# Kernel optimization log

Hardware: AMD Instinct MI355X
Metric: run time of the kernel (lower is better)

Reference implementation:

```python
import jax, jax.numpy as jnp
import numpy as np

B, T, D = 4096, 64, 64
NE, NR = 100000, 100
PREFIXES = ["kgi", "ddp", "kgp", "ddo", "kgi1", "ddp1", "kgp1", "ddo1"]


def setup_inputs() -> dict:
    key = jax.random.key(0)
    keys = iter(jax.random.split(key, 80))
    inp = {"items": jax.random.randint(next(keys), (B,), 0, NE)}
    for p in PREFIXES:
        for s, hi in [("h0", NE), ("h1", NE), ("r0", NR), ("r1", NR), ("t0", NE), ("t1", NE)]:
            inp[p + "_" + s] = jax.random.randint(next(keys), (B, T), 0, hi)
    inp["embeddings_0"] = jax.random.normal(next(keys), (B, D), jnp.float32)
    inp["embeddings_1"] = jax.random.normal(next(keys), (B, D), jnp.float32)
    inp["entity_emb"] = jax.random.normal(next(keys), (NE, D), jnp.float32) * 0.05
    inp["relation_emb"] = jax.random.normal(next(keys), (NR, D), jnp.float32) * 0.05
    inp["W1"] = jax.random.normal(next(keys), (2 * D, D), jnp.float32) * (1.0 / np.sqrt(2 * D))
    inp["W2"] = jax.random.normal(next(keys), (D, 1), jnp.float32) * (1.0 / np.sqrt(D))
    return inp


def _knowledge_attention(h_set, path, t, W1, W2):
    # h_set, path, t: [B, T, D]; tiny sigmoid MLP -> softmax over triples -> weighted sum
    x = jnp.concatenate([h_set, path], axis=-1)                 # [B, T, 2D]
    att = jax.nn.sigmoid(jax.nn.sigmoid(x @ W1) @ W2)[..., 0]   # [B, T]
    att = jax.nn.softmax(att, axis=-1)
    return jnp.einsum('bt,btd->bd', att, t)                     # [B, D]


def _layers(E, R, W1, W2, h0, h1, r0, r1, t0, t1, init):
    # Faithful to the original n_layer=2 loop:
    #  i=0: h=E[h0], p=R[r0], t=E[t0];  i=1: h=E[h0]+E[h1], p=R[r0]*R[r1], t=E[t1]
    embs = [init]
    h, p = E[h0], R[r0]
    embs.append(_knowledge_attention(h, p, E[t0], W1, W2))
    h = h + E[h1]
    p = p * R[r1]
    embs.append(_knowledge_attention(h, p, E[t1], W1, W2))
    return embs


def reference(items, kgi_h0, kgi_h1, kgi_r0, kgi_r1, kgi_t0, kgi_t1,
              ddp_h0, ddp_h1, ddp_r0, ddp_r1, ddp_t0, ddp_t1,
              kgp_h0, kgp_h1, kgp_r0, kgp_r1, kgp_t0, kgp_t1,
              ddo_h0, ddo_h1, ddo_r0, ddo_r1, ddo_t0, ddo_t1,
              kgi1_h0, kgi1_h1, kgi1_r0, kgi1_r1, kgi1_t0, kgi1_t1,
              ddp1_h0, ddp1_h1, ddp1_r0, ddp1_r1, ddp1_t0, ddp1_t1,
              kgp1_h0, kgp1_h1, kgp1_r0, kgp1_r1, kgp1_t0, kgp1_t1,
              ddo1_h0, ddo1_h1, ddo1_r0, ddo1_r1, ddo1_t0, ddo1_t1,
              embeddings_0, embeddings_1, entity_emb, relation_emb, W1, W2):
    E, R = entity_emb, relation_emb
    kg = _layers(E, R, W1, W2, kgi_h0, kgi_h1, kgi_r0, kgi_r1, kgi_t0, kgi_t1, E[kgi_h0].mean(1))
    ddi = _layers(E, R, W1, W2, ddp_h0, ddp_h1, ddp_r0, ddp_r1, ddp_t0, ddp_t1, E[items])
    kgp = _layers(E, R, W1, W2, kgp_h0, kgp_h1, kgp_r0, kgp_r1, kgp_t0, kgp_t1, E[kgp_h0].mean(1))
    ddo = _layers(E, R, W1, W2, ddo_h0, ddo_h1, ddo_r0, ddo_r1, ddo_t0, ddo_t1, E[ddo_h0].mean(1))
    kg1 = _layers(E, R, W1, W2, kgi1_h0, kgi1_h1, kgi1_r0, kgi1_r1, kgi1_t0, kgi1_t1, E[kgi1_h0].mean(1))
    ddi1 = _layers(E, R, W1, W2, ddp1_h0, ddp1_h1, ddp1_r0, ddp1_r1, ddp1_t0, ddp1_t1, E[ddp1_h0].mean(1))
    kgp1 = _layers(E, R, W1, W2, kgp1_h0, kgp1_h1, kgp1_r0, kgp1_r1, kgp1_t0, kgp1_t1, E[kgp1_h0].mean(1))
    ddo1 = _layers(E, R, W1, W2, ddo1_h0, ddo1_h1, ddo1_r0, ddo1_r1, ddo1_t0, ddo1_t1, E[ddo1_h0].mean(1))
    del ddo, kg1, kgp1  # dead in the original score due to list aliasing/overwrite in predict()
    # predict() with agg='concat'; original aliases ddi_origin_embeddings = ddi_embeddings,
    drug_kg = [jnp.concatenate([kg[i], ddi[i]], -1) for i in range(3)]       # [B, 2D]
    drug_kg2 = [jnp.concatenate([kgp[i], ddi[i]], -1) for i in range(3)]     # [B, 2D]
    drug_d = [jnp.concatenate([ddi1[i], ddo1[i]], -1) for i in range(3)]     # [B, 2D]
    e_u = jnp.concatenate([drug_kg[2], drug_kg[1], drug_kg[0]], -1)          # [B, 6D]
    e_p_u = jnp.concatenate([drug_kg2[2], drug_kg2[1], drug_kg2[0]], -1)     # [B, 6D]
    e_i = jnp.concatenate([drug_d[2], drug_d[1], drug_d[0]], -1)             # [B, 6D]
    e1 = jnp.concatenate([e_u, e_p_u], -1)                                   # [B, 12D]
    e2 = jnp.concatenate([e_i, e_i], -1)                                     # [B, 12D] (e_p_i aliases e_i)
    scores = jax.nn.sigmoid(jnp.sum(e1 * e2, axis=-1))                       # [B]
    return scores
```

## Files before the change

### kernel.cpp

```cpp
#include <hip/hip_runtime.h>

#define BATCH 4096
#define NE 100000

typedef __attribute__((ext_vector_type(8))) short bf16x8;
typedef __attribute__((ext_vector_type(4))) float f32x4;

union U4 { uint4 u4; bf16x8 v; };

struct GPtrs {
    const int* h0[5]; const int* h1[5];
    const int* r0[5]; const int* r1[5];
    const int* t0[5]; const int* t1[5];
};

__device__ __forceinline__ unsigned trunc2(float lo, float hi){
    return __builtin_amdgcn_perm(__float_as_uint(hi), __float_as_uint(lo), 0x07060302u);
}
__device__ __forceinline__ float bflo(unsigned u){ return __uint_as_float(u << 16); }
__device__ __forceinline__ float bfhi(unsigned u){ return __uint_as_float(u & 0xFFFF0000u); }
__device__ __forceinline__ float bf2f(unsigned short h){ return __uint_as_float(((unsigned)h) << 16); }
__device__ __forceinline__ unsigned addw(unsigned x, unsigned y){
    return trunc2(bflo(x)+bflo(y), bfhi(x)+bfhi(y));
}
__device__ __forceinline__ unsigned mulw(unsigned x, unsigned y){
    return trunc2(bflo(x)*bflo(y), bfhi(x)*bfhi(y));
}
__device__ __forceinline__ float sigm(float x){ return __builtin_amdgcn_rcpf(1.0f + __expf(-x)); }

__global__ __launch_bounds__(256)
void prep_kernel(const float* __restrict__ E, const float* __restrict__ R,
                 const float* __restrict__ W1,
                 unsigned short* __restrict__ ebf, unsigned short* __restrict__ rbf,
                 uint4* __restrict__ w1pk)
{
    const int EC = (NE*64)/8;
    const int RC = (100*64)/8;
    const int WC = 1024;
    int stride = gridDim.x * blockDim.x;
    for (int c = blockIdx.x*blockDim.x + threadIdx.x; c < EC + RC + WC; c += stride) {
        if (c < EC + RC) {
            const float* src; unsigned short* dst;
            if (c < EC) { src = E + c*8;      dst = ebf + c*8; }
            else        { src = R + (c-EC)*8; dst = rbf + (c-EC)*8; }
            float4 a = *(const float4*)src;
            float4 b = *(const float4*)(src + 4);
            uint4 o;
            o.x = trunc2(a.x,a.y); o.y = trunc2(a.z,a.w);
            o.z = trunc2(b.x,b.y); o.w = trunc2(b.z,b.w);
            *(uint4*)dst = o;
        } else {
            int c2   = c - (EC + RC);
            int frag = c2 >> 6;
            int ln   = c2 & 63;
            int row  = (frag >> 2)*16 + (ln & 15);
            int kp0  = (frag & 3)*16 + 4*(ln >> 4);
            uint4 o;
            o.x = trunc2(W1[(2*kp0    )*64 + row], W1[(2*kp0 + 1)*64 + row]);
            o.y = trunc2(W1[(2*kp0 + 2)*64 + row], W1[(2*kp0 + 3)*64 + row]);
            o.z = trunc2(W1[(2*kp0 + 4)*64 + row], W1[(2*kp0 + 5)*64 + row]);
            o.w = trunc2(W1[(2*kp0 + 6)*64 + row], W1[(2*kp0 + 7)*64 + row]);
            w1pk[c2] = o;
        }
    }
}

__global__ __launch_bounds__(256, 2)
void group_kernel(GPtrs gp, const int* __restrict__ items,
                  const float* __restrict__ E,
                  const unsigned short* __restrict__ ebf,
                  const unsigned short* __restrict__ rbf,
                  const uint4* __restrict__ w1pk, const float* __restrict__ W2,
                  float* __restrict__ ws)
{
    const int g    = blockIdx.y;
    const int b    = blockIdx.x;
    const int tid  = threadIdx.x;
    const int lane = tid & 63;
    const int wv   = tid >> 6;

    __shared__ uint4 wlds[1024];
    __shared__ float red_log[64];
    __shared__ float red_pv[4][64];

    {
        wlds[tid      ] = w1pk[tid      ];
        wlds[tid + 256] = w1pk[tid + 256];
        wlds[tid + 512] = w1pk[tid + 512];
        wlds[tid + 768] = w1pk[tid + 768];
    }

    const int tcol = lane & 15;
    const int q    = lane >> 4;
    const int q4   = q * 4;
    const int t_   = wv*16 + tcol;

    int vh0 = gp.h0[g][b*64 + lane];
    int vh1 = gp.h1[g][b*64 + lane];
    int vr0 = gp.r0[g][b*64 + lane];
    int vr1 = gp.r1[g][b*64 + lane];
    int vt0 = gp.t0[g][b*64 + lane];
    int vt1 = gp.t1[g][b*64 + lane];

    __syncthreads();

    if (g == 1) {
        if (wv == 0) ws[((g*3 + 0)*BATCH + b)*64 + lane] = E[items[b]*64 + lane];
    } else {
        float o0 = 0.f, o1 = 0.f, o2 = 0.f, o3 = 0.f;
        #pragma unroll
        for (int u = 0; u < 16; u += 4) {
            int t = wv*16 + u;
            int r0_ = __shfl(vh0, t,   64);
            int r1_ = __shfl(vh0, t+1, 64);
            int r2_ = __shfl(vh0, t+2, 64);
            int r3_ = __shfl(vh0, t+3, 64);
            o0 += bf2f(ebf[r0_*64 + lane]); o1 += bf2f(ebf[r1_*64 + lane]);
            o2 += bf2f(ebf[r2_*64 + lane]); o3 += bf2f(ebf[r3_*64 + lane]);
        }
        red_pv[wv][lane] = ((o0+o1)+(o2+o3));
        __syncthreads();
        if (wv == 0)
            ws[((g*3 + 0)*BATCH + b)*64 + lane] =
                (red_pv[0][lane]+red_pv[1][lane]+red_pv[2][lane]+red_pv[3][lane]) * (1.0f/64.0f);
    }

    U4 f0, f1, f2, f3;
    {
        int hr0 = __shfl(vh0, t_, 64);
        int pr0 = __shfl(vr0, t_, 64);
        const uint4* hp = (const uint4*)(ebf + hr0*64);
        const uint4* pp = (const uint4*)(rbf + pr0*64);
        f0.u4 = hp[q];
        f1.u4 = hp[4 + q];
        f2.u4 = pp[q];
        f3.u4 = pp[4 + q];
    }

    #pragma unroll
    for (int L = 0; L < 2; ++L) {
        if (L == 1) {
            int hr1 = __shfl(vh1, t_, 64);
            int pr1 = __shfl(vr1, t_, 64);
            const uint4* hq = (const uint4*)(ebf + hr1*64);
            const uint4* pq = (const uint4*)(rbf + pr1*64);
            uint4 x0 = hq[q], x1 = hq[4+q], y0 = pq[q], y1 = pq[4+q];
            f0.u4 = make_uint4(addw(f0.u4.x,x0.x), addw(f0.u4.y,x0.y),
                               addw(f0.u4.z,x0.z), addw(f0.u4.w,x0.w));
            f1.u4 = make_uint4(addw(f1.u4.x,x1.x), addw(f1.u4.y,x1.y),
                               addw(f1.u4.z,x1.z), addw(f1.u4.w,x1.w));
            f2.u4 = make_uint4(mulw(f2.u4.x,y0.x), mulw(f2.u4.y,y0.y),
                               mulw(f2.u4.z,y0.z), mulw(f2.u4.w,y0.w));
            f3.u4 = make_uint4(mulw(f3.u4.x,y1.x), mulw(f3.u4.y,y1.y),
                               mulw(f3.u4.z,y1.z), mulw(f3.u4.w,y1.w));
        }

        float pt = 0.f;
        #pragma unroll
        for (int jt = 0; jt < 4; ++jt) {
            U4 wf0, wf1, wf2, wf3;
            wf0.u4 = wlds[(jt*4 + 0)*64 + lane];
            wf1.u4 = wlds[(jt*4 + 1)*64 + lane];
            wf2.u4 = wlds[(jt*4 + 2)*64 + lane];
            wf3.u4 = wlds[(jt*4 + 3)*64 + lane];
            f32x4 acc = {0.f, 0.f, 0.f, 0.f};
            acc = __builtin_amdgcn_mfma_f32_16x16x32_bf16(wf0.v, f0.v, acc, 0,0,0);
            acc = __builtin_amdgcn_mfma_f32_16x16x32_bf16(wf1.v, f1.v, acc, 0,0,0);
            acc = __builtin_amdgcn_mfma_f32_16x16x32_bf16(wf2.v, f2.v, acc, 0,0,0);
            acc = __builtin_amdgcn_mfma_f32_16x16x32_bf16(wf3.v, f3.v, acc, 0,0,0);
            float4 w2v = *(const float4*)(W2 + jt*16 + q4);
            pt += sigm(acc[0])*w2v.x + sigm(acc[1])*w2v.y
                + sigm(acc[2])*w2v.z + sigm(acc[3])*w2v.w;
        }
        pt += __shfl_xor(pt, 16, 64);
        pt += __shfl_xor(pt, 32, 64);
        if (lane < 16) red_log[wv*16 + lane] = sigm(pt);
        __syncthreads();

        float e = __expf(red_log[lane]);
        float den = e;
        #pragma unroll
        for (int m = 32; m > 0; m >>= 1) den += __shfl_xor(den, m, 64);
        float att = e * __builtin_amdgcn_rcpf(den);

        int vt = (L == 0) ? vt0 : vt1;
        float o0 = 0.f, o1 = 0.f, o2 = 0.f, o3 = 0.f;
        #pragma unroll
        for (int u = 0; u < 16; u += 4) {
            int t = wv*16 + u;
            int r0_ = __shfl(vt, t,   64);
            int r1_ = __shfl(vt, t+1, 64);
            int r2_ = __shfl(vt, t+2, 64);
            int r3_ = __shfl(vt, t+3, 64);
            float a0_ = __shfl(att, t,   64);
            float a1_ = __shfl(att, t+1, 64);
            float a2_ = __shfl(att, t+2, 64);
            float a3_ = __shfl(att, t+3, 64);
            o0 = fmaf(a0_, bf2f(ebf[r0_*64 + lane]), o0);
            o1 = fmaf(a1_, bf2f(ebf[r1_*64 + lane]), o1);
            o2 = fmaf(a2_, bf2f(ebf[r2_*64 + lane]), o2);
            o3 = fmaf(a3_, bf2f(ebf[r3_*64 + lane]), o3);
        }
        red_pv[wv][lane] = (o0+o1)+(o2+o3);
        __syncthreads();
        if (wv == 0)
            ws[((g*3 + 1 + L)*BATCH + b)*64 + lane] =
                red_pv[0][lane]+red_pv[1][lane]+red_pv[2][lane]+red_pv[3][lane];
    }
}

__launch_bounds__(256, 4)
__global__ void combine_kernel(const float* __restrict__ ws, float* __restrict__ out)
{
    const int tid  = threadIdx.x;
    const int lane = tid & 63;
    const int wv   = tid >> 6;
    const int b    = blockIdx.x*4 + wv;
    float acc = 0.f;
    #pragma unroll
    for (int i = 0; i < 3; ++i) {
        float kg   = ws[((0*3+i)*BATCH + b)*64 + lane];
        float ddi  = ws[((1*3+i)*BATCH + b)*64 + lane];
        float kgp  = ws[((2*3+i)*BATCH + b)*64 + lane];
        float ddi1 = ws[((3*3+i)*BATCH + b)*64 + lane];
        float ddo1 = ws[((4*3+i)*BATCH + b)*64 + lane];
        acc += (kg + kgp)*ddi1 + 2.0f*ddi*ddo1;
    }
    #pragma unroll
    for (int m = 32; m > 0; m >>= 1) acc += __shfl_xor(acc, m, 64);
    if (lane == 0) out[b] = 1.0f/(1.0f + __expf(-acc));
}

extern "C" void kernel_launch(void* const* d_in, const int* in_sizes, int n_in,
                              void* d_out, int out_size, void* d_ws, size_t ws_size,
                              hipStream_t stream)
{
    const int gbase[5] = {1, 7, 13, 31, 43};
    GPtrs gp;
    for (int g = 0; g < 5; ++g) {
        gp.h0[g] = (const int*)d_in[gbase[g]+0];
        gp.h1[g] = (const int*)d_in[gbase[g]+1];
        gp.r0[g] = (const int*)d_in[gbase[g]+2];
        gp.r1[g] = (const int*)d_in[gbase[g]+3];
        gp.t0[g] = (const int*)d_in[gbase[g]+4];
        gp.t1[g] = (const int*)d_in[gbase[g]+5];
    }
    const int*   items = (const int*)d_in[0];
    const float* E     = (const float*)d_in[51];
    const float* R     = (const float*)d_in[52];
    const float* W1    = (const float*)d_in[53];
    const float* W2    = (const float*)d_in[54];

    float*          ws  = (float*)d_ws;
    unsigned short* ebf = (unsigned short*)((char*)d_ws + 15728640);
    unsigned short* rbf = (unsigned short*)((char*)d_ws + 15728640 + 12800000);
    uint4*          w1pk= (uint4*)((char*)d_ws + 15728640 + 12800000 + 12800 + 64);

    prep_kernel<<<1024, 256, 0, stream>>>(E, R, W1, ebf, rbf, w1pk);
    dim3 grid(BATCH, 5);
    group_kernel<<<grid, 256, 0, stream>>>(gp, items, E, ebf, rbf, w1pk, W2, ws);
    combine_kernel<<<BATCH/4, 256, 0, stream>>>(ws, (float*)d_out);
}
```

Measured before the change: 177.6 us.

## Process four batch rows per block to amortize W1 LDS staging

```diff
diff --git a/kernel.cpp b/kernel.cpp
--- a/kernel.cpp
+++ b/kernel.cpp
@@ -2,6 +2,7 @@
 
 #define BATCH 4096
 #define NE 100000
+#define NC 4
 
 typedef __attribute__((ext_vector_type(8))) short bf16x8;
 typedef __attribute__((ext_vector_type(4))) float f32x4;
@@ -74,88 +75,104 @@
                   float* __restrict__ ws)
 {
     const int g    = blockIdx.y;
-    const int b    = blockIdx.x;
+    const int b0   = blockIdx.x*NC;
     const int tid  = threadIdx.x;
     const int lane = tid & 63;
     const int wv   = tid >> 6;
 
     __shared__ uint4 wlds[1024];
-    __shared__ float red_log[64];
-    __shared__ float red_pv[4][64];
-
-    {
-        wlds[tid      ] = w1pk[tid      ];
-        wlds[tid + 256] = w1pk[tid + 256];
-        wlds[tid + 512] = w1pk[tid + 512];
-        wlds[tid + 768] = w1pk[tid + 768];
-    }
+    __shared__ float red_log[NC][64];
+    __shared__ float red_pv[NC][4][64];
+
+    wlds[tid      ] = w1pk[tid      ];
+    wlds[tid + 256] = w1pk[tid + 256];
+    wlds[tid + 512] = w1pk[tid + 512];
+    wlds[tid + 768] = w1pk[tid + 768];
 
     const int tcol = lane & 15;
     const int q    = lane >> 4;
     const int q4   = q * 4;
     const int t_   = wv*16 + tcol;
 
-    int vh0 = gp.h0[g][b*64 + lane];
-    int vh1 = gp.h1[g][b*64 + lane];
-    int vr0 = gp.r0[g][b*64 + lane];
-    int vr1 = gp.r1[g][b*64 + lane];
-    int vt0 = gp.t0[g][b*64 + lane];
-    int vt1 = gp.t1[g][b*64 + lane];
+    int vh0[NC], vh1[NC], vr0[NC], vr1[NC], vt0[NC], vt1[NC];
+    #pragma unroll
+    for (int c = 0; c < NC; ++c) {
+        int bb = b0 + c;
+        vh0[c] = gp.h0[g][bb*64 + lane];
+        vh1[c] = gp.h1[g][bb*64 + lane];
+        vr0[c] = gp.r0[g][bb*64 + lane];
+        vr1[c] = gp.r1[g][bb*64 + lane];
+        vt0[c] = gp.t0[g][bb*64 + lane];
+        vt1[c] = gp.t1[g][bb*64 + lane];
+    }
 
     __syncthreads();
 
     if (g == 1) {
-        if (wv == 0) ws[((g*3 + 0)*BATCH + b)*64 + lane] = E[items[b]*64 + lane];
+        int bb = b0 + wv;
+        ws[((g*3 + 0)*BATCH + bb)*64 + lane] = E[items[bb]*64 + lane];
     } else {
-        float o0 = 0.f, o1 = 0.f, o2 = 0.f, o3 = 0.f;
-        #pragma unroll
-        for (int u = 0; u < 16; u += 4) {
-            int t = wv*16 + u;
-            int r0_ = __shfl(vh0, t,   64);
-            int r1_ = __shfl(vh0, t+1, 64);
-            int r2_ = __shfl(vh0, t+2, 64);
-            int r3_ = __shfl(vh0, t+3, 64);
-            o0 += bf2f(ebf[r0_*64 + lane]); o1 += bf2f(ebf[r1_*64 + lane]);
-            o2 += bf2f(ebf[r2_*64 + lane]); o3 += bf2f(ebf[r3_*64 + lane]);
-        }
-        red_pv[wv][lane] = ((o0+o1)+(o2+o3));
-        __syncthreads();
-        if (wv == 0)
-            ws[((g*3 + 0)*BATCH + b)*64 + lane] =
-                (red_pv[0][lane]+red_pv[1][lane]+red_pv[2][lane]+red_pv[3][lane]) * (1.0f/64.0f);
-    }
-
-    U4 f0, f1, f2, f3;
-    {
-        int hr0 = __shfl(vh0, t_, 64);
-        int pr0 = __shfl(vr0, t_, 64);
-        const uint4* hp = (const uint4*)(ebf + hr0*64);
-        const uint4* pp = (const uint4*)(rbf + pr0*64);
-        f0.u4 = hp[q];
-        f1.u4 = hp[4 + q];
-        f2.u4 = pp[q];
-        f3.u4 = pp[4 + q];
+        #pragma unroll
+        for (int c = 0; c < NC; ++c) {
+            float o0 = 0.f, o1 = 0.f, o2 = 0.f, o3 = 0.f;
+            #pragma unroll
+            for (int u = 0; u < 16; u += 4) {
+                int t = wv*16 + u;
+                int r0_ = __shfl(vh0[c], t,   64);
+                int r1_ = __shfl(vh0[c], t+1, 64);
+                int r2_ = __shfl(vh0[c], t+2, 64);
+                int r3_ = __shfl(vh0[c], t+3, 64);
+                o0 += bf2f(ebf[r0_*64 + lane]); o1 += bf2f(ebf[r1_*64 + lane]);
+                o2 += bf2f(ebf[r2_*64 + lane]); o3 += bf2f(ebf[r3_*64 + lane]);
+            }
+            red_pv[c][wv][lane] = (o0+o1)+(o2+o3);
+        }
+        __syncthreads();
+        {
+            int bb = b0 + wv;
+            ws[((g*3 + 0)*BATCH + bb)*64 + lane] =
+                (red_pv[wv][0][lane]+red_pv[wv][1][lane]+
+                 red_pv[wv][2][lane]+red_pv[wv][3][lane]) * (1.0f/64.0f);
+        }
+    }
+
+    U4 f[NC][4];
+    #pragma unroll
+    for (int c = 0; c < NC; ++c) {
+        int hr = __shfl(vh0[c], t_, 64);
+        int pr = __shfl(vr0[c], t_, 64);
+        const uint4* hp = (const uint4*)(ebf + hr*64);
+        const uint4* pp = (const uint4*)(rbf + pr*64);
+        f[c][0].u4 = hp[q];
+        f[c][1].u4 = hp[4 + q];
+        f[c][2].u4 = pp[q];
+        f[c][3].u4 = pp[4 + q];
     }
 
     #pragma unroll
     for (int L = 0; L < 2; ++L) {
         if (L == 1) {
-            int hr1 = __shfl(vh1, t_, 64);
-            int pr1 = __shfl(vr1, t_, 64);
-            const uint4* hq = (const uint4*)(ebf + hr1*64);
-            const uint4* pq = (const uint4*)(rbf + pr1*64);
-            uint4 x0 = hq[q], x1 = hq[4+q], y0 = pq[q], y1 = pq[4+q];
-            f0.u4 = make_uint4(addw(f0.u4.x,x0.x), addw(f0.u4.y,x0.y),
-                               addw(f0.u4.z,x0.z), addw(f0.u4.w,x0.w));
-            f1.u4 = make_uint4(addw(f1.u4.x,x1.x), addw(f1.u4.y,x1.y),
-                               addw(f1.u4.z,x1.z), addw(f1.u4.w,x1.w));
-            f2.u4 = make_uint4(mulw(f2.u4.x,y0.x), mulw(f2.u4.y,y0.y),
-                               mulw(f2.u4.z,y0.z), mulw(f2.u4.w,y0.w));
-            f3.u4 = make_uint4(mulw(f3.u4.x,y1.x), mulw(f3.u4.y,y1.y),
-                               mulw(f3.u4.z,y1.z), mulw(f3.u4.w,y1.w));
-        }
-
-        float pt = 0.f;
+            #pragma unroll
+            for (int c = 0; c < NC; ++c) {
+                int hr = __shfl(vh1[c], t_, 64);
+                int pr = __shfl(vr1[c], t_, 64);
+                const uint4* hq = (const uint4*)(ebf + hr*64);
+                const uint4* pq = (const uint4*)(rbf + pr*64);
+                uint4 x0 = hq[q], x1 = hq[4+q], y0 = pq[q], y1 = pq[4+q];
+                f[c][0].u4 = make_uint4(addw(f[c][0].u4.x,x0.x), addw(f[c][0].u4.y,x0.y),
+                                        addw(f[c][0].u4.z,x0.z), addw(f[c][0].u4.w,x0.w));
+                f[c][1].u4 = make_uint4(addw(f[c][1].u4.x,x1.x), addw(f[c][1].u4.y,x1.y),
+                                        addw(f[c][1].u4.z,x1.z), addw(f[c][1].u4.w,x1.w));
+                f[c][2].u4 = make_uint4(mulw(f[c][2].u4.x,y0.x), mulw(f[c][2].u4.y,y0.y),
+                                        mulw(f[c][2].u4.z,y0.z), mulw(f[c][2].u4.w,y0.w));
+                f[c][3].u4 = make_uint4(mulw(f[c][3].u4.x,y1.x), mulw(f[c][3].u4.y,y1.y),
+                                        mulw(f[c][3].u4.z,y1.z), mulw(f[c][3].u4.w,y1.w));
+            }
+        }
+
+        float pt[NC];
+        #pragma unroll
+        for (int c = 0; c < NC; ++c) pt[c] = 0.f;
         #pragma unroll
         for (int jt = 0; jt < 4; ++jt) {
             U4 wf0, wf1, wf2, wf3;
@@ -163,49 +180,67 @@
             wf1.u4 = wlds[(jt*4 + 1)*64 + lane];
             wf2.u4 = wlds[(jt*4 + 2)*64 + lane];
             wf3.u4 = wlds[(jt*4 + 3)*64 + lane];
-            f32x4 acc = {0.f, 0.f, 0.f, 0.f};
-            acc = __builtin_amdgcn_mfma_f32_16x16x32_bf16(wf0.v, f0.v, acc, 0,0,0);
-            acc = __builtin_amdgcn_mfma_f32_16x16x32_bf16(wf1.v, f1.v, acc, 0,0,0);
-            acc = __builtin_amdgcn_mfma_f32_16x16x32_bf16(wf2.v, f2.v, acc, 0,0,0);
-            acc = __builtin_amdgcn_mfma_f32_16x16x32_bf16(wf3.v, f3.v, acc, 0,0,0);
             float4 w2v = *(const float4*)(W2 + jt*16 + q4);
-            pt += sigm(acc[0])*w2v.x + sigm(acc[1])*w2v.y
-                + sigm(acc[2])*w2v.z + sigm(acc[3])*w2v.w;
-        }
-        pt += __shfl_xor(pt, 16, 64);
-        pt += __shfl_xor(pt, 32, 64);
-        if (lane < 16) red_log[wv*16 + lane] = sigm(pt);
-        __syncthreads();
-
-        float e = __expf(red_log[lane]);
-        float den = e;
-        #pragma unroll
-        for (int m = 32; m > 0; m >>= 1) den += __shfl_xor(den, m, 64);
-        float att = e * __builtin_amdgcn_rcpf(den);
-
-        int vt = (L == 0) ? vt0 : vt1;
-        float o0 = 0.f, o1 = 0.f, o2 = 0.f, o3 = 0.f;
-        #pragma unroll
-        for (int u = 0; u < 16; u += 4) {
-            int t = wv*16 + u;
-            int r0_ = __shfl(vt, t,   64);
-            int r1_ = __shfl(vt, t+1, 64);
-            int r2_ = __shfl(vt, t+2, 64);
-            int r3_ = __shfl(vt, t+3, 64);
-            float a0_ = __shfl(att, t,   64);
-            float a1_ = __shfl(att, t+1, 64);
-            float a2_ = __shfl(att, t+2, 64);
-            float a3_ = __shfl(att, t+3, 64);
-            o0 = fmaf(a0_, bf2f(ebf[r0_*64 + lane]), o0);
-            o1 = fmaf(a1_, bf2f(ebf[r1_*64 + lane]), o1);
-            o2 = fmaf(a2_, bf2f(ebf[r2_*64 + lane]), o2);
-            o3 = fmaf(a3_, bf2f(ebf[r3_*64 + lane]), o3);
-        }
-        red_pv[wv][lane] = (o0+o1)+(o2+o3);
-        __syncthreads();
-        if (wv == 0)
-            ws[((g*3 + 1 + L)*BATCH + b)*64 + lane] =
-                red_pv[0][lane]+red_pv[1][lane]+red_pv[2][lane]+red_pv[3][lane];
+            #pragma unroll
+            for (int c = 0; c < NC; ++c) {
+                f32x4 acc = {0.f, 0.f, 0.f, 0.f};
+                acc = __builtin_amdgcn_mfma_f32_16x16x32_bf16(wf0.v, f[c][0].v, acc, 0,0,0);
+                acc = __builtin_amdgcn_mfma_f32_16x16x32_bf16(wf1.v, f[c][1].v, acc, 0,0,0);
+                acc = __builtin_amdgcn_mfma_f32_16x16x32_bf16(wf2.v, f[c][2].v, acc, 0,0,0);
+                acc = __builtin_amdgcn_mfma_f32_16x16x32_bf16(wf3.v, f[c][3].v, acc, 0,0,0);
+                pt[c] += sigm(acc[0])*w2v.x + sigm(acc[1])*w2v.y
+                       + sigm(acc[2])*w2v.z + sigm(acc[3])*w2v.w;
+            }
+        }
+        #pragma unroll
+        for (int c = 0; c < NC; ++c) {
+            float p = pt[c];
+            p += __shfl_xor(p, 16, 64);
+            p += __shfl_xor(p, 32, 64);
+            if (lane < 16) red_log[c][wv*16 + lane] = sigm(p);
+        }
+        __syncthreads();
+
+        float att[NC];
+        #pragma unroll
+        for (int c = 0; c < NC; ++c) {
+            float e = __expf(red_log[c][lane]);
+            float d = e;
+            #pragma unroll
+            for (int m = 32; m > 0; m >>= 1) d += __shfl_xor(d, m, 64);
+            att[c] = e * __builtin_amdgcn_rcpf(d);
+        }
+
+        #pragma unroll
+        for (int c = 0; c < NC; ++c) {
+            int vt = (L == 0) ? vt0[c] : vt1[c];
+            float o0 = 0.f, o1 = 0.f, o2 = 0.f, o3 = 0.f;
+            #pragma unroll
+            for (int u = 0; u < 16; u += 4) {
+                int t = wv*16 + u;
+                int r0_ = __shfl(vt, t,   64);
+                int r1_ = __shfl(vt, t+1, 64);
+                int r2_ = __shfl(vt, t+2, 64);
+                int r3_ = __shfl(vt, t+3, 64);
+                float a0_ = __shfl(att[c], t,   64);
+                float a1_ = __shfl(att[c], t+1, 64);
+                float a2_ = __shfl(att[c], t+2, 64);
+                float a3_ = __shfl(att[c], t+3, 64);
+                o0 = fmaf(a0_, bf2f(ebf[r0_*64 + lane]), o0);
+                o1 = fmaf(a1_, bf2f(ebf[r1_*64 + lane]), o1);
+                o2 = fmaf(a2_, bf2f(ebf[r2_*64 + lane]), o2);
+                o3 = fmaf(a3_, bf2f(ebf[r3_*64 + lane]), o3);
+            }
+            red_pv[c][wv][lane] = (o0+o1)+(o2+o3);
+        }
+        __syncthreads();
+        {
+            int bb = b0 + wv;
+            ws[((g*3 + 1 + L)*BATCH + bb)*64 + lane] =
+                red_pv[wv][0][lane]+red_pv[wv][1][lane]+
+                red_pv[wv][2][lane]+red_pv[wv][3][lane];
+        }
+        __syncthreads();
     }
 }
 
@@ -257,7 +292,7 @@
     uint4*          w1pk= (uint4*)((char*)d_ws + 15728640 + 12800000 + 12800 + 64);
 
     prep_kernel<<<1024, 256, 0, stream>>>(E, R, W1, ebf, rbf, w1pk);
-    dim3 grid(BATCH, 5);
+    dim3 grid(BATCH/NC, 5);
     group_kernel<<<grid, 256, 0, stream>>>(gp, items, E, ebf, rbf, w1pk, W2, ws);
     combine_kernel<<<BATCH/4, 256, 0, stream>>>(ws, (float*)d_out);
 }
```

Measured after the change: 330.5 us. +86.1%, slower.
